# Optimization experiments

Measured on AMD Instinct MI355X. Metric: run time of the kernel, lower is better.

The kernel has to match this reference:

```python
import jax, jax.numpy as jnp
import numpy as np

B, D, T, H, C = 65536, 1024, 16, 128, 10


def setup_inputs() -> dict:
    key = jax.random.key(0)
    k1, k2, k3, k4, k5, k6 = jax.random.split(key, 6)
    x = jax.random.normal(k1, (B, D), dtype=jnp.float32)
    task_id = jax.random.randint(k2, (B,), 0, T, dtype=jnp.int32)
    # per-task head params (torch nn.Linear init scale ~ 1/sqrt(fan_in))
    W1 = jax.random.normal(k3, (T, D, H), dtype=jnp.float32) / np.sqrt(D)
    b1 = jax.random.normal(k4, (T, H), dtype=jnp.float32) * 0.01
    W2 = jax.random.normal(k5, (T, H, C), dtype=jnp.float32) / np.sqrt(H)
    b2 = jax.random.normal(k6, (T, C), dtype=jnp.float32) * 0.01
    return {"x": x, "task_id": task_id, "W1": W1, "b1": b1, "W2": W2, "b2": b2}


def reference(x, task_id, W1, b1, W2, b2):
    # Dense dispatch: run every head on every sample as one big GEMM
    # (x @ [T*H] concatenated weights), then select each sample's task head.
    # Same math as the torch per-task mask/gather/scatter loop (eval mode,
    # dropout is identity).
    h = jax.nn.relu(jnp.einsum('bd,tdh->bth', x, W1) + b1)      # [B,T,H]
    logits_all = jnp.einsum('bth,thc->btc', h, W2) + b2          # [B,T,C]
    # gather the row for each sample's task_id
    logits = jnp.take_along_axis(
        logits_all, task_id[:, None, None].astype(jnp.int32), axis=1
    ).squeeze(1)                                                 # [B,C]
    return logits
```

## Files before the change

### kernel.cpp

```cpp
#include <hip/hip_runtime.h>
#include <hip/hip_bf16.h>

#define TASKS 16
#define DIM 1024
#define HID 128
#define NCLS 10
#define NB 65536
#define BM 128
#define NTILES (NB / BM + TASKS)

#define WS_RIDX 64
#define WS_W1S  (WS_RIDX + 16 * NB)

typedef __attribute__((ext_vector_type(8))) short bf16x8;
typedef __attribute__((ext_vector_type(4))) float f32x4;
typedef __attribute__((ext_vector_type(2))) unsigned u32x2;

__device__ __forceinline__ unsigned short f2bf(float f) {
    union { __hip_bfloat16 h; unsigned short s; } u; u.h = __float2bfloat16(f); return u.s;
}

__device__ __forceinline__ void glds16(const void* gsrc, void* ldst) {
    __builtin_amdgcn_global_load_lds(
        (const __attribute__((address_space(1))) unsigned*)gsrc,
        (__attribute__((address_space(3))) unsigned*)ldst, 16, 0, 0);
}

__global__ __launch_bounds__(256) void k_prep(const int* __restrict__ tid_arr,
                                              const float* __restrict__ W1,
                                              const float* __restrict__ W2,
                                              int* __restrict__ ws) {
    const int blk = blockIdx.x, tid = threadIdx.x;
    if (blk < 256) {
        __shared__ int l[TASKS], base[TASKS];
        if (tid < TASKS) l[tid] = 0;
        __syncthreads();
        const int i = blk * 256 + tid;
        const int t = tid_arr[i];
        const int rank = atomicAdd(&l[t], 1);
        __syncthreads();
        if (tid < TASKS && l[tid] > 0) base[tid] = atomicAdd(&ws[tid], l[tid]);
        __syncthreads();
        ws[WS_RIDX + t * NB + base[t] + rank] = i;
    } else if (blk < 768) {
        const int idx = blk - 256;
        const int t = idx >> 5, kt = idx & 31;
        __shared__ float ld[32 * 132];
        const float* src = W1 + ((size_t)t * DIM + kt * 32) * HID;
        #pragma unroll
        for (int r = 0; r < 16; ++r) {
            const int fl = r * 256 + tid;
            ld[(fl >> 7) * 132 + (fl & 127)] = src[fl];
        }
        __syncthreads();
        char* dst = (char*)((short*)(ws + WS_W1S) + ((size_t)(t * 32 + kt) << 12));
        #pragma unroll
        for (int g = 0; g < 2; ++g) {
            const int p = tid * 32 + g * 16;
            const int kslot = p >> 11, col = (p >> 4) & 127;
            bf16x8 v;
            #pragma unroll
            for (int j = 0; j < 8; ++j)
                v[j] = (short)f2bf(ld[(kslot * 8 + j) * 132 + col]);
            *(bf16x8*)(dst + p) = v;
        }
    } else {
        const int t = blk - 768;
        short* W2t = (short*)(ws + WS_W1S) + ((size_t)TASKS * 32 * 4096);
        #pragma unroll
        for (int i = 0; i < 8; ++i) {
            const int o = i * 256 + tid, c = o >> 7, h = o & 127;
            const float v = (c < NCLS) ? W2[((size_t)t * HID + h) * NCLS + c] : 0.f;
            W2t[((size_t)t * 16 + c) * HID + h] = (short)f2bf(v);
        }
    }
}

__global__ __launch_bounds__(512, 6) void k_main(
    const float* __restrict__ x, const float* __restrict__ b1,
    const float* __restrict__ b2, const int* __restrict__ ws,
    float* __restrict__ out)
{
    __shared__ __align__(16) short smem[16384];
    __shared__ int ridx[BM];

    const int* tot = ws;
    const int* rowIdx = ws + WS_RIDX;
    const short* W1s = (const short*)(ws + WS_W1S);
    const short* W2t = W1s + ((size_t)TASKS * 32 * 4096);

    const int w = (blockIdx.x & 7) * (NTILES / 8) + (blockIdx.x >> 3);

    int t = -1, m = 0, tileInT = 0;
    {
        int accT = 0;
        for (int k = 0; k < TASKS; ++k) {
            const int c = tot[k], nt = (c + BM - 1) >> 7;
            if (t < 0 && w < accT + nt) {
                t = k; tileInT = w - accT;
                m = c - tileInT * BM; if (m > BM) m = BM;
            }
            accT += nt;
        }
    }
    if (t < 0) return;

    const int tid = threadIdx.x;
    if (tid < BM) {
        const int rr = tid < m ? tid : m - 1;
        ridx[tid] = rowIdx[t * NB + tileInT * BM + rr];
    }
    __syncthreads();

    const int lane = tid & 63, wv = tid >> 6;
    const int lg = lane >> 4, lr = lane & 15;
    const int rh = wv & 1, cq = wv >> 1;
    const int wrow = rh * 64, wcol = cq * 32;

    const float* gpA[2];
    unsigned wbA[2];
    #pragma unroll
    for (int j = 0; j < 2; ++j) {
        const int row = wv * 16 + j * 8 + (lane >> 3);
        gpA[j] = x + ((size_t)ridx[row] << 10) + (lane & 7) * 4;
        wbA[j] = ((unsigned)((lane & 7) >> 1)) * 2048 + row * 16 + (lane & 1) * 8;
    }
    const char* w1sT = (const char*)W1s + ((size_t)t << 18);

    f32x4 a8[2];
    f32x4 acc[4][2] = {};

    auto LOADA = [&](int kt) {
        #pragma unroll
        for (int j = 0; j < 2; ++j) a8[j] = *(const f32x4*)(gpA[j] + kt * 32);
    };
    auto WRITEA = [&](int buf) {
        char* ab = (char*)smem + buf * 16384;
        #pragma unroll
        for (int j = 0; j < 2; ++j) {
            u32x2 pk;
            pk[0] = ((unsigned)f2bf(a8[j][1]) << 16) | (unsigned)f2bf(a8[j][0]);
            pk[1] = ((unsigned)f2bf(a8[j][3]) << 16) | (unsigned)f2bf(a8[j][2]);
            *(u32x2*)(ab + wbA[j]) = pk;
        }
    };
    auto ISSUEB = [&](int buf, int kt) {
        const char* src = w1sT + ((size_t)kt << 13) + wv * 1024 + lane * 16;
        char* dst = (char*)smem + buf * 16384 + 8192 + wv * 1024;
        glds16(src, dst);
    };
    auto COMPUTE = [&](int buf) {
        const char* ab = (const char*)smem + buf * 16384;
        const char* bb = ab + 8192;
        bf16x8 af[4], bfr[2];
        #pragma unroll
        for (int rf = 0; rf < 4; ++rf)
            af[rf] = *(const bf16x8*)(ab + lg * 2048 + (wrow + rf * 16 + lr) * 16);
        #pragma unroll
        for (int cf = 0; cf < 2; ++cf)
            bfr[cf] = *(const bf16x8*)(bb + lg * 2048 + (wcol + cf * 16 + lr) * 16);
        #pragma unroll
        for (int rf = 0; rf < 4; ++rf)
            #pragma unroll
            for (int cf = 0; cf < 2; ++cf)
                acc[rf][cf] = __builtin_amdgcn_mfma_f32_16x16x32_bf16(af[rf], bfr[cf], acc[rf][cf], 0, 0, 0);
    };

    LOADA(0);
    ISSUEB(0, 0);
    WRITEA(0);
    LOADA(1);
    asm volatile("s_waitcnt vmcnt(2) lgkmcnt(0)" ::: "memory");
    __builtin_amdgcn_s_barrier();
    __builtin_amdgcn_sched_barrier(0);

    #pragma unroll 2
    for (int kt = 0; kt < 32; ++kt) {
        const int buf = kt & 1;
        ISSUEB(buf ^ 1, kt + 1 < 32 ? kt + 1 : 31);
        WRITEA(buf ^ 1);
        LOADA(kt + 2 < 32 ? kt + 2 : 31);
        COMPUTE(buf);
        asm volatile("s_waitcnt vmcnt(2) lgkmcnt(0)" ::: "memory");
        __builtin_amdgcn_s_barrier();
        __builtin_amdgcn_sched_barrier(0);
    }
    __syncthreads();

    short* hl = smem;
    #pragma unroll
    for (int cf = 0; cf < 2; ++cf) {
        const int col = wcol + cf * 16 + lr;
        const float b1v = b1[t * HID + col];
        #pragma unroll
        for (int rf = 0; rf < 4; ++rf)
            #pragma unroll
            for (int q = 0; q < 4; ++q) {
                const int row = wrow + rf * 16 + lg * 4 + q;
                const float hv = fmaxf(acc[rf][cf][q] + b1v, 0.f);
                *(unsigned short*)((char*)hl + row * 256 +
                    (((col >> 3) ^ (row & 7)) << 4) + (col & 7) * 2) = f2bf(hv);
            }
    }
    __syncthreads();

    const int row2 = wv * 16 + lr;
    f32x4 acc2 = {};
    #pragma unroll
    for (int ks = 0; ks < 4; ++ks) {
        bf16x8 bvv = *(const bf16x8*)(W2t + (((size_t)t * 16 + lr) << 7) + ks * 32 + lg * 8);
        bf16x8 avv = *(const bf16x8*)((const char*)hl + row2 * 256 +
                         (((ks * 4 + lg) ^ (row2 & 7)) << 4));
        acc2 = __builtin_amdgcn_mfma_f32_16x16x32_bf16(avv, bvv, acc2, 0, 0, 0);
    }
    if (lr < NCLS) {
        const float b2v = b2[t * NCLS + lr];
        #pragma unroll
        for (int q = 0; q < 4; ++q) {
            const int row = wv * 16 + lg * 4 + q;
            if (row < m) out[(size_t)ridx[row] * NCLS + lr] = acc2[q] + b2v;
        }
    }
}

extern "C" void kernel_launch(void* const* d_in, const int* in_sizes, int n_in,
                              void* d_out, int out_size, void* d_ws, size_t ws_size,
                              hipStream_t stream) {
    (void)in_sizes; (void)n_in; (void)out_size; (void)ws_size;
    const float* x       = (const float*)d_in[0];
    const int*   task_id = (const int*)d_in[1];
    const float* W1      = (const float*)d_in[2];
    const float* b1      = (const float*)d_in[3];
    const float* W2      = (const float*)d_in[4];
    const float* b2      = (const float*)d_in[5];
    float* out = (float*)d_out;
    int* ws = (int*)d_ws;
    hipMemsetAsync(ws, 0, 64, stream);
    k_prep<<<784, 256, 0, stream>>>(task_id, W1, W2, ws);
    k_main<<<NTILES, 512, 0, stream>>>(x, b1, b2, ws, out);
}
```

Before: 78.13 us.

## Deepen K-step to 128 and load W1 fragments directly into registers

The main GEMM loop now processes 128 K-elements per iteration (8 iterations instead of 32), with a 64 KB double-buffered LDS tile for the converted x rows. W1 fragments are read straight from global memory into registers instead of staging through LDS with global_load_lds, and the hand-placed waitcnt/sched barriers are replaced by plain __syncthreads. The aim is fewer barriers and more memory requests in flight per iteration. In exchange it uses more registers and LDS per block (launch bounds drop from 6 to 4 blocks), so occupancy falls.

Measured after the change: 84.60 us. +8.3%, slower.

```diff
diff --git a/kernel.cpp b/kernel.cpp
--- a/kernel.cpp
+++ b/kernel.cpp
@@ -18,12 +18,6 @@
 
 __device__ __forceinline__ unsigned short f2bf(float f) {
     union { __hip_bfloat16 h; unsigned short s; } u; u.h = __float2bfloat16(f); return u.s;
-}
-
-__device__ __forceinline__ void glds16(const void* gsrc, void* ldst) {
-    __builtin_amdgcn_global_load_lds(
-        (const __attribute__((address_space(1))) unsigned*)gsrc,
-        (__attribute__((address_space(3))) unsigned*)ldst, 16, 0, 0);
 }
 
 __global__ __launch_bounds__(256) void k_prep(const int* __restrict__ tid_arr,
@@ -76,12 +70,12 @@
     }
 }
 
-__global__ __launch_bounds__(512, 6) void k_main(
+__global__ __launch_bounds__(512, 4) void k_main(
     const float* __restrict__ x, const float* __restrict__ b1,
     const float* __restrict__ b2, const int* __restrict__ ws,
     float* __restrict__ out)
 {
-    __shared__ __align__(16) short smem[16384];
+    __shared__ __align__(16) char smem[65536];
     __shared__ int ridx[BM];
 
     const int* tot = ws;
@@ -117,77 +111,77 @@
     const int rh = wv & 1, cq = wv >> 1;
     const int wrow = rh * 64, wcol = cq * 32;
 
-    const float* gpA[2];
-    unsigned wbA[2];
+    const int ar = wv * 16 + (lane >> 3);
+    const int pc = lane & 7;
+    const float* srcA0 = x + ((size_t)ridx[ar] << 10) + pc * 4;
+    const float* srcA1 = x + ((size_t)ridx[ar + 8] << 10) + pc * 4;
+    const char* w1sT = (const char*)W1s + ((size_t)t << 18);
+    const unsigned bbase = (unsigned)(lg * 2048 + ((wcol + lr) << 4));
+
+    f32x4 aR[8];
+    bf16x8 bR[8];
+    f32x4 acc[4][2] = {};
+
+    auto LOADA = [&](int kt) {
+        #pragma unroll
+        for (int j = 0; j < 4; ++j) {
+            aR[j]     = *(const f32x4*)(srcA0 + kt * 128 + j * 32);
+            aR[4 + j] = *(const f32x4*)(srcA1 + kt * 128 + j * 32);
+        }
+    };
+    auto ISSUEB = [&](int kt) {
+        #pragma unroll
+        for (int s = 0; s < 4; ++s)
+            #pragma unroll
+            for (int cf = 0; cf < 2; ++cf)
+                bR[s * 2 + cf] = *(const bf16x8*)(
+                    w1sT + (size_t)(kt * 4 + s) * 8192 + bbase + cf * 256);
+    };
+    auto CVTWRITE = [&](int buf) {
+        char* ab = smem + buf * 32768;
+        #pragma unroll
+        for (int j = 0; j < 4; ++j) {
+            const unsigned base = (unsigned)((j * 4 + (pc >> 1)) * 2048 + (pc & 1) * 8);
+            u32x2 p0, p1;
+            p0[0] = ((unsigned)f2bf(aR[j][1]) << 16) | f2bf(aR[j][0]);
+            p0[1] = ((unsigned)f2bf(aR[j][3]) << 16) | f2bf(aR[j][2]);
+            p1[0] = ((unsigned)f2bf(aR[4 + j][1]) << 16) | f2bf(aR[4 + j][0]);
+            p1[1] = ((unsigned)f2bf(aR[4 + j][3]) << 16) | f2bf(aR[4 + j][2]);
+            *(u32x2*)(ab + base + ar * 16) = p0;
+            *(u32x2*)(ab + base + (ar + 8) * 16) = p1;
+        }
+    };
+    auto COMPUTE = [&](int buf) {
+        const char* ab = smem + buf * 32768;
+        #pragma unroll
+        for (int s = 0; s < 4; ++s) {
+            const int koff = (s * 4 + lg) * 2048;
+            bf16x8 af[4];
+            #pragma unroll
+            for (int rf = 0; rf < 4; ++rf)
+                af[rf] = *(const bf16x8*)(ab + koff + ((wrow + rf * 16 + lr) << 4));
+            #pragma unroll
+            for (int rf = 0; rf < 4; ++rf) {
+                acc[rf][0] = __builtin_amdgcn_mfma_f32_16x16x32_bf16(af[rf], bR[s * 2],     acc[rf][0], 0, 0, 0);
+                acc[rf][1] = __builtin_amdgcn_mfma_f32_16x16x32_bf16(af[rf], bR[s * 2 + 1], acc[rf][1], 0, 0, 0);
+            }
+        }
+    };
+
+    LOADA(0);
+    CVTWRITE(0);
+    __syncthreads();
+
     #pragma unroll
-    for (int j = 0; j < 2; ++j) {
-        const int row = wv * 16 + j * 8 + (lane >> 3);
-        gpA[j] = x + ((size_t)ridx[row] << 10) + (lane & 7) * 4;
-        wbA[j] = ((unsigned)((lane & 7) >> 1)) * 2048 + row * 16 + (lane & 1) * 8;
-    }
-    const char* w1sT = (const char*)W1s + ((size_t)t << 18);
-
-    f32x4 a8[2];
-    f32x4 acc[4][2] = {};
-
-    auto LOADA = [&](int kt) {
-        #pragma unroll
-        for (int j = 0; j < 2; ++j) a8[j] = *(const f32x4*)(gpA[j] + kt * 32);
-    };
-    auto WRITEA = [&](int buf) {
-        char* ab = (char*)smem + buf * 16384;
-        #pragma unroll
-        for (int j = 0; j < 2; ++j) {
-            u32x2 pk;
-            pk[0] = ((unsigned)f2bf(a8[j][1]) << 16) | (unsigned)f2bf(a8[j][0]);
-            pk[1] = ((unsigned)f2bf(a8[j][3]) << 16) | (unsigned)f2bf(a8[j][2]);
-            *(u32x2*)(ab + wbA[j]) = pk;
-        }
-    };
-    auto ISSUEB = [&](int buf, int kt) {
-        const char* src = w1sT + ((size_t)kt << 13) + wv * 1024 + lane * 16;
-        char* dst = (char*)smem + buf * 16384 + 8192 + wv * 1024;
-        glds16(src, dst);
-    };
-    auto COMPUTE = [&](int buf) {
-        const char* ab = (const char*)smem + buf * 16384;
-        const char* bb = ab + 8192;
-        bf16x8 af[4], bfr[2];
-        #pragma unroll
-        for (int rf = 0; rf < 4; ++rf)
-            af[rf] = *(const bf16x8*)(ab + lg * 2048 + (wrow + rf * 16 + lr) * 16);
-        #pragma unroll
-        for (int cf = 0; cf < 2; ++cf)
-            bfr[cf] = *(const bf16x8*)(bb + lg * 2048 + (wcol + cf * 16 + lr) * 16);
-        #pragma unroll
-        for (int rf = 0; rf < 4; ++rf)
-            #pragma unroll
-            for (int cf = 0; cf < 2; ++cf)
-                acc[rf][cf] = __builtin_amdgcn_mfma_f32_16x16x32_bf16(af[rf], bfr[cf], acc[rf][cf], 0, 0, 0);
-    };
-
-    LOADA(0);
-    ISSUEB(0, 0);
-    WRITEA(0);
-    LOADA(1);
-    asm volatile("s_waitcnt vmcnt(2) lgkmcnt(0)" ::: "memory");
-    __builtin_amdgcn_s_barrier();
-    __builtin_amdgcn_sched_barrier(0);
-
-    #pragma unroll 2
-    for (int kt = 0; kt < 32; ++kt) {
-        const int buf = kt & 1;
-        ISSUEB(buf ^ 1, kt + 1 < 32 ? kt + 1 : 31);
-        WRITEA(buf ^ 1);
-        LOADA(kt + 2 < 32 ? kt + 2 : 31);
-        COMPUTE(buf);
-        asm volatile("s_waitcnt vmcnt(2) lgkmcnt(0)" ::: "memory");
-        __builtin_amdgcn_s_barrier();
-        __builtin_amdgcn_sched_barrier(0);
-    }
-    __syncthreads();
-
-    short* hl = smem;
+    for (int kt = 0; kt < 8; ++kt) {
+        ISSUEB(kt);
+        LOADA(kt + 1 < 8 ? kt + 1 : 7);
+        COMPUTE(kt & 1);
+        CVTWRITE((kt + 1) & 1);
+        __syncthreads();
+    }
+
+    char* hl = smem;
     #pragma unroll
     for (int cf = 0; cf < 2; ++cf) {
         const int col = wcol + cf * 16 + lr;
@@ -198,7 +192,7 @@
             for (int q = 0; q < 4; ++q) {
                 const int row = wrow + rf * 16 + lg * 4 + q;
                 const float hv = fmaxf(acc[rf][cf][q] + b1v, 0.f);
-                *(unsigned short*)((char*)hl + row * 256 +
+                *(unsigned short*)(hl + row * 256 +
                     (((col >> 3) ^ (row & 7)) << 4) + (col & 7) * 2) = f2bf(hv);
             }
     }
@@ -209,8 +203,7 @@
     #pragma unroll
     for (int ks = 0; ks < 4; ++ks) {
         bf16x8 bvv = *(const bf16x8*)(W2t + (((size_t)t * 16 + lr) << 7) + ks * 32 + lg * 8);
-        bf16x8 avv = *(const bf16x8*)((const char*)hl + row2 * 256 +
-                         (((ks * 4 + lg) ^ (row2 & 7)) << 4));
+        bf16x8 avv = *(const bf16x8*)(hl + row2 * 256 + (((ks * 4 + lg) ^ (row2 & 7)) << 4));
         acc2 = __builtin_amdgcn_mfma_f32_16x16x32_bf16(avv, bvv, acc2, 0, 0, 0);
     }
     if (lr < NCLS) {
```
